# Performance work log

Hardware: AMD Instinct MI355X
Metric: run time of the kernel (lower is better)

The kernel has to match this reference:

```python
import jax, jax.numpy as jnp
import numpy as np

L, D, H, DK, S, B = 6, 1024, 16, 64, 512, 8
DFF = 4 * D
NEG = -1.0e9


def layer_norm(x, g, b, eps=1e-5):
    mu = jnp.mean(x, axis=-1, keepdims=True)
    var = jnp.var(x, axis=-1, keepdims=True)
    return (x - mu) * jax.lax.rsqrt(var + eps) * g + b


def setup_inputs() -> dict:
    key = jax.random.key(0)
    ks = jax.random.split(key, 16)
    s = 0.02
    inp = {
        "x": jax.random.normal(ks[0], (B, S, D), jnp.float32),
        "mask": jax.random.bernoulli(ks[1], 0.1, (B, S, S)),
        "relation": jax.random.normal(ks[2], (B, S, S), jnp.float32) * 0.1,
        # per-layer params (stacked over L)
        "Wq": jax.random.normal(ks[3], (L, D, H * DK), jnp.float32) * s,
        "Wk": jax.random.normal(ks[4], (L, D, H * DK), jnp.float32) * s,
        "Wv": jax.random.normal(ks[5], (L, D, H * DK), jnp.float32) * s,
        "Wo": jax.random.normal(ks[6], (L, H * DK, D), jnp.float32) * s,
        "bo": jnp.zeros((L, D), jnp.float32),
        "ln_g": jnp.ones((L, D), jnp.float32),   # EncoderLayer.norm (shared pre-attn / pre-FFN)
        "ln_b": jnp.zeros((L, D), jnp.float32),
        "ln2_g": jnp.ones((L, D), jnp.float32),  # AttSubLayerv2.norm
        "ln2_b": jnp.zeros((L, D), jnp.float32),
        "W1": jax.random.normal(ks[7], (L, D, DFF), jnp.float32) * s,
        "b1": jnp.zeros((L, DFF), jnp.float32),
        "W2": jax.random.normal(ks[8], (L, DFF, D), jnp.float32) * s,
        "b2": jnp.zeros((L, D), jnp.float32),
        "lnf_g": jnp.ones((D,), jnp.float32),    # Encoder.norm
        "lnf_b": jnp.zeros((D,), jnp.float32),
    }
    return inp


def reference(x, mask, relation, Wq, Wk, Wv, Wo, bo, ln_g, ln_b, ln2_g, ln2_b,
              W1, b1, W2, b2, lnf_g, lnf_b):
    # dropout layers run in eval mode (identity)
    scale = 1.0 / jnp.sqrt(jnp.asarray(DK, x.dtype))
    h = x
    attns = []
    for l in range(L):
        q_in = layer_norm(h, ln_g[l], ln_b[l])
        # AttSubLayerv2
        def proj(W):
            return jnp.einsum('bsd,de->bse', q_in, W).reshape(h.shape[0], -1, H, DK).transpose(0, 2, 1, 3)
        Q, K, V = proj(Wq[l]), proj(Wk[l]), proj(Wv[l])  # [B,H,S,DK]
        qk = jnp.einsum('bhqd,bhkd->bhqk', Q, K)
        scores = jnp.einsum('bhqk,bkn->bhqn', qk, relation) * scale
        scores = jnp.where(mask[:, None], NEG, scores)
        p = jax.nn.softmax(scores, axis=-1)  # [B,H,S,S]
        att = jnp.einsum('bhqk,bhkd->bhqd', p, V).transpose(0, 2, 1, 3).reshape(h.shape[0], -1, H * DK)
        att = att @ Wo[l] + bo[l]
        att_out = layer_norm(att + q_in, ln2_g[l], ln2_b[l])
        h = h + att_out
        # FFN (pre-norm with shared EncoderLayer norm)
        f = layer_norm(h, ln_g[l], ln_b[l])
        h = h + (jax.nn.relu(f @ W1[l] + b1[l]) @ W2[l] + b2[l])
        attns.append(p)
    out = layer_norm(h, lnf_g, lnf_b)
    return out, jnp.stack(attns)
```

## Files before the change

kernel.cpp:

```cpp
#include <hip/hip_runtime.h>
#include <hip/hip_bf16.h>
#include <stdint.h>

#define LL 6
#define DD 1024
#define HH 16
#define DKK 64
#define SS 512
#define BB 8
#define DFF_ 4096
#define BS (BB*SS)
#define NEGV -1.0e9f

typedef __attribute__((ext_vector_type(8))) short short8;
typedef __attribute__((ext_vector_type(4))) float f32x4;
typedef __attribute__((ext_vector_type(4))) unsigned short ushort4v;

static __device__ __forceinline__ float bf2f(unsigned short u){
  union { unsigned int i; float f; } v; v.i = ((unsigned int)u)<<16; return v.f;
}
static __device__ __forceinline__ unsigned short f2bf(float f){
  union { float f; unsigned int i; } v; v.f=f;
  unsigned int r = v.i + 0x7fff + ((v.i>>16)&1);
  return (unsigned short)(r>>16);
}

static __device__ __forceinline__ void gload16(const void* g, void* l){
  __builtin_amdgcn_global_load_lds((const __attribute__((address_space(1))) unsigned int*)g,
                                   (__attribute__((address_space(3))) unsigned int*)l, 16, 0, 0);
}

struct TrDesc { const float* in; unsigned short* out; long is1,is2,os1,os2; int ldin,ldout,zd,gx,gy; };
struct TrPack { TrDesc d[7]; int cum[8]; };

__global__ void __launch_bounds__(256) tr_multi_k(TrPack P)
{
  __shared__ float t[32][33];
  int bid=blockIdx.x, di=0;
  #pragma unroll
  for(int k=1;k<7;k++) if(bid>=P.cum[k]) di=k;
  TrDesc dd=P.d[di];
  int local=bid-P.cum[di];
  int bx=local%dd.gx; int rest=local/dd.gx;
  int by=rest%dd.gy; int z=rest/dd.gy;
  int z1=z/dd.zd, z2=z%dd.zd;
  const float* ip=dd.in+z1*dd.is1+z2*dd.is2;
  unsigned short* op=dd.out+z1*dd.os1+z2*dd.os2;
  int r0=by*32, c0=bx*32;
  int tx=threadIdx.x, ty=threadIdx.y;
  #pragma unroll
  for(int i=0;i<4;i++)
    t[ty+i*8][tx] = ip[(long)(r0+ty+i*8)*dd.ldin + c0+tx];
  __syncthreads();
  #pragma unroll
  for(int i=0;i<4;i++)
    op[(long)(c0+ty+i*8)*dd.ldout + r0+tx] = f2bf(t[tx][ty+i*8]);
}

__global__ void __launch_bounds__(256) maskpack_k(const int* __restrict__ mask, unsigned* __restrict__ mb)
{
  int idx = blockIdx.x*256 + threadIdx.x;
  int row = idx>>4, w = idx&15;
  const int* mp = mask + (long)row*SS + w*32;
  unsigned v=0;
  #pragma unroll
  for(int i=0;i<32;i++) v |= (mp[i]!=0) ? (1u<<i) : 0u;
  mb[idx]=v;
}

__global__ void __launch_bounds__(256) ln_k(const float* __restrict__ src,
    const float* __restrict__ gw, const float* __restrict__ bw,
    float* __restrict__ outf, unsigned short* __restrict__ outb,
    const float* __restrict__ resid)
{
  long row=blockIdx.x;
  float4 v=((const float4*)(src+row*DD))[threadIdx.x];
  float s=v.x+v.y+v.z+v.w;
  float s2=v.x*v.x+v.y*v.y+v.z*v.z+v.w*v.w;
  #pragma unroll
  for(int o=32;o;o>>=1){ s+=__shfl_xor(s,o); s2+=__shfl_xor(s2,o); }
  __shared__ float red[8];
  int wid=threadIdx.x>>6, lane=threadIdx.x&63;
  if(lane==0){ red[wid]=s; red[4+wid]=s2; }
  __syncthreads();
  s=red[0]+red[1]+red[2]+red[3];
  s2=red[4]+red[5]+red[6]+red[7];
  float mu=s*(1.f/DD);
  float rstd=rsqrtf(s2*(1.f/DD)-mu*mu+1e-5f);
  int c=threadIdx.x*4;
  float4 g4=*(const float4*)(gw+c), b4=*(const float4*)(bw+c);
  float4 o;
  o.x=(v.x-mu)*rstd*g4.x+b4.x;
  o.y=(v.y-mu)*rstd*g4.y+b4.y;
  o.z=(v.z-mu)*rstd*g4.z+b4.z;
  o.w=(v.w-mu)*rstd*g4.w+b4.w;
  if(resid){
    float4 r4=((const float4*)(resid+row*DD))[threadIdx.x];
    o.x+=r4.x; o.y+=r4.y; o.z+=r4.z; o.w+=r4.w;
  }
  if(outf) ((float4*)(outf+row*DD))[threadIdx.x]=o;
  if(outb){
    uint2 pk;
    pk.x=(unsigned)f2bf(o.x)|((unsigned)f2bf(o.y)<<16);
    pk.y=(unsigned)f2bf(o.z)|((unsigned)f2bf(o.w)<<16);
    ((uint2*)(outb+row*DD))[threadIdx.x]=pk;
  }
}

__global__ void __launch_bounds__(256) ln2_k(const float* __restrict__ src,
    const float* __restrict__ resid,
    const float* __restrict__ g2, const float* __restrict__ b2,
    const float* __restrict__ g1, const float* __restrict__ b1,
    float* __restrict__ outf, unsigned short* __restrict__ outb)
{
  long row=blockIdx.x;
  int wid=threadIdx.x>>6, lane=threadIdx.x&63, c=threadIdx.x*4;
  __shared__ float red[8];
  float4 v=((const float4*)(src+row*DD))[threadIdx.x];
  float s=v.x+v.y+v.z+v.w;
  float s2=v.x*v.x+v.y*v.y+v.z*v.z+v.w*v.w;
  #pragma unroll
  for(int o=32;o;o>>=1){ s+=__shfl_xor(s,o); s2+=__shfl_xor(s2,o); }
  if(lane==0){ red[wid]=s; red[4+wid]=s2; }
  __syncthreads();
  s=red[0]+red[1]+red[2]+red[3];
  s2=red[4]+red[5]+red[6]+red[7];
  float mu=s*(1.f/DD);
  float rstd=rsqrtf(s2*(1.f/DD)-mu*mu+1e-5f);
  float4 g4=*(const float4*)(g2+c), b4=*(const float4*)(b2+c);
  float4 r4=((const float4*)(resid+row*DD))[threadIdx.x];
  float4 o;
  o.x=(v.x-mu)*rstd*g4.x+b4.x+r4.x;
  o.y=(v.y-mu)*rstd*g4.y+b4.y+r4.y;
  o.z=(v.z-mu)*rstd*g4.z+b4.z+r4.z;
  o.w=(v.w-mu)*rstd*g4.w+b4.w+r4.w;
  ((float4*)(outf+row*DD))[threadIdx.x]=o;
  s=o.x+o.y+o.z+o.w;
  s2=o.x*o.x+o.y*o.y+o.z*o.z+o.w*o.w;
  #pragma unroll
  for(int of=32;of;of>>=1){ s+=__shfl_xor(s,of); s2+=__shfl_xor(s2,of); }
  __syncthreads();
  if(lane==0){ red[wid]=s; red[4+wid]=s2; }
  __syncthreads();
  s=red[0]+red[1]+red[2]+red[3];
  s2=red[4]+red[5]+red[6]+red[7];
  mu=s*(1.f/DD);
  rstd=rsqrtf(s2*(1.f/DD)-mu*mu+1e-5f);
  g4=*(const float4*)(g1+c); b4=*(const float4*)(b1+c);
  uint2 pk;
  pk.x=(unsigned)f2bf((o.x-mu)*rstd*g4.x+b4.x)|((unsigned)f2bf((o.y-mu)*rstd*g4.y+b4.y)<<16);
  pk.y=(unsigned)f2bf((o.z-mu)*rstd*g4.z+b4.z)|((unsigned)f2bf((o.w-mu)*rstd*g4.w+b4.w)<<16);
  ((uint2*)(outb+row*DD))[threadIdx.x]=pk;
}

struct GemmP {
  const unsigned short* A; long sA1; int ldA;
  const unsigned short* B; long sB1; int ldB;
  float* outF; unsigned short* outB; long sO1; int ldO;
  const float* bias;
  const float* residF; int ldR;
  const unsigned short* residB;
  unsigned short *kt, *vt;
  int K, relu;
};

template<int MODE>
__global__ void __launch_bounds__(512,2) gemm8_k(GemmP p)
{
  constexpr int BM=128, BN=128, BK=64;
  constexpr int BUFE=(BM+BN)*BK;
  constexpr int FN=2;
  constexpr int WNT=32;
  __shared__ __align__(16) unsigned short smem[4*BUFE];
  const int tid=threadIdx.x, lane=tid&63, wid=tid>>6;
  const int wr=wid>>2, wc=wid&3;
  const int lr=lane&15, lk=(lane>>4)*8;
  const int m0=blockIdx.y*BM, n0=blockIdx.x*BN;
  const int z=blockIdx.z;
  const unsigned short* Ap=p.A+(long)z*p.sA1;
  const unsigned short* Bp=p.B+(long)z*p.sB1;
  const int NT=p.K/BK;

  const int sr8 = lane>>3;
  const int scol = ((lane&7) ^ sr8) << 3;

  #define STAGE8(T,BI) { \
    const long kb_=(long)(T)*BK; \
    unsigned short* As_=smem+(BI)*BUFE; \
    unsigned short* Bs_=As_+BM*BK; \
    _Pragma("unroll") \
    for(int L=0;L<2;L++){ \
      int r_=L*64+wid*8+sr8; \
      gload16(Ap+(long)(m0+r_)*p.ldA+kb_+scol, As_+L*4096+wid*512); \
    } \
    _Pragma("unroll") \
    for(int L=0;L<2;L++){ \
      int r_=L*64+wid*8+sr8; \
      gload16(Bp+(long)(n0+r_)*p.ldB+kb_+scol, Bs_+L*4096+wid*512); \
    } }

  f32x4 acc[4][FN];
  #pragma unroll
  for(int m=0;m<4;m++)
    #pragma unroll
    for(int n=0;n<FN;n++) acc[m][n]=(f32x4){0.f,0.f,0.f,0.f};

  STAGE8(0,0);
  STAGE8(1,1);
  __syncthreads();

  const int xr = (lr&7)<<3;
  for(int t=0;t<NT;t+=2){
    if(t+2<NT) STAGE8(t+2,(t+2)&3);
    if(t+3<NT) STAGE8(t+3,(t+3)&3);
    #pragma unroll
    for(int u=0;u<2;u++){
      const unsigned short* As=smem+((t+u)&3)*BUFE;
      const unsigned short* Bs=As+BM*BK;
      #pragma unroll
      for(int kk=0;kk<2;kk++){
        short8 a[4], b[FN];
        #pragma unroll
        for(int m=0;m<4;m++)
          a[m]=*(const short8*)(As + (wr*64+m*16+lr)*BK + ((kk*32+lk)^xr));
        #pragma unroll
        for(int n=0;n<FN;n++)
          b[n]=*(const short8*)(Bs + (wc*WNT+n*16+lr)*BK + ((kk*32+lk)^xr));
        __builtin_amdgcn_s_setprio(1);
        #pragma unroll
        for(int m=0;m<4;m++)
          #pragma unroll
          for(int n=0;n<FN;n++)
            acc[m][n]=__builtin_amdgcn_mfma_f32_16x16x32_bf16(a[m],b[n],acc[m][n],0,0,0);
        __builtin_amdgcn_s_setprio(0);
      }
    }
    __syncthreads();
  }
  #undef STAGE8

  const int rl=(lane>>4)*4;
  if(MODE==1){
    int sec = n0>>10;
    #pragma unroll
    for(int m=0;m<4;m++){
      int gr0 = m0 + wr*64 + m*16 + rl;
      int b = gr0>>9, s0 = gr0&511;
      #pragma unroll
      for(int n=0;n<FN;n++){
        int gc = n0 + wc*WNT + n*16 + lr;
        if(sec==0){
          #pragma unroll
          for(int r=0;r<4;r++)
            p.outB[(long)(gr0+r)*1024 + gc] = f2bf(acc[m][n][r]);
        } else {
          unsigned short* dst = sec==1 ? p.kt : p.vt;
          int hh=(gc>>6)&15, d=gc&63;
          ushort4v pk;
          pk.x=f2bf(acc[m][n][0]); pk.y=f2bf(acc[m][n][1]);
          pk.z=f2bf(acc[m][n][2]); pk.w=f2bf(acc[m][n][3]);
          *(ushort4v*)(dst + (((long)b*HH+hh)*DKK+d)*SS + s0) = pk;
        }
      }
    }
  } else {
    #pragma unroll
    for(int m=0;m<4;m++){
      int gr0 = m0 + wr*64 + m*16 + rl;
      #pragma unroll
      for(int n=0;n<FN;n++){
        int gc = n0 + wc*WNT + n*16 + lr;
        float bv = p.bias ? p.bias[gc] : 0.f;
        #pragma unroll
        for(int r=0;r<4;r++){
          long ro=(long)(gr0+r);
          float val=acc[m][n][r]+bv;
          if(p.relu) val=fmaxf(val,0.f);
          if(p.residF) val += p.residF[ro*(long)p.ldR+gc];
          if(p.residB) val += bf2f(p.residB[ro*(long)p.ldR+gc]);
          long oo = (long)z*p.sO1 + ro*(long)p.ldO+gc;
          if(p.outF) p.outF[oo]=val;
          if(p.outB) p.outB[oo]=f2bf(val);
        }
      }
    }
  }
}

template<int MODE>
static inline void launch_gemm8(GemmP& p,int M,int N,int Z,hipStream_t s){
  gemm8_k<MODE><<<dim3(N/128,M/128,Z),dim3(512),0,s>>>(p);
}

__global__ void __launch_bounds__(512) att_k(const unsigned short* __restrict__ Qb,
    const unsigned short* __restrict__ KRT, float* __restrict__ pout,
    const unsigned* __restrict__ maskb, const unsigned short* __restrict__ Vt,
    unsigned short* __restrict__ attb)
{
  constexpr int BM=128, BK=32, NT=512;
  constexpr int FM=4, FN=8;
  __shared__ __align__(16) char smem[49152];
  unsigned short* As = (unsigned short*)smem;
  unsigned short* Bs = (unsigned short*)(smem+8192);
  unsigned short* Ps = (unsigned short*)smem;
  unsigned short* Vs = (unsigned short*)(smem+32768);
  __shared__ float redmx[BM][4];
  __shared__ float redsm[BM][4];
  int bh = blockIdx.y; int b = bh>>4, h = bh&15;
  const unsigned short* Ap = Qb + (long)b*SS*1024 + h*64;
  const unsigned short* Bp = KRT + (long)b*SS*1024 + h*64;
  int m0 = blockIdx.x*BM;
  int tid=threadIdx.x, lane=tid&63, wid=tid>>6;
  int wr=wid>>2, wc=wid&3;
  f32x4 acc[FM][FN];
  #pragma unroll
  for(int i=0;i<FM;i++)
    #pragma unroll
    for(int j=0;j<FN;j++) acc[i][j]=(f32x4){0.f,0.f,0.f,0.f};
  const int lr=lane&15, lk=(lane>>4)*8;
  for(int k0=0;k0<DKK;k0+=BK){
    { int v=tid;
      gload16(Ap + (long)(m0+(v>>2))*1024 + k0 + (v&3)*8, As + (wid*64)*8); }
    #pragma unroll
    for(int r=0;r<4;r++){
      int v=r*NT+tid;
      gload16(Bp + (long)(v>>2)*1024 + k0 + (v&3)*8, Bs + (r*NT+wid*64)*8);
    }
    __syncthreads();
    short8 af[FM], bfr[FN];
    #pragma unroll
    for(int i=0;i<FM;i++) af[i]=*(const short8*)(As + (wr*64+i*16+lr)*BK + lk);
    #pragma unroll
    for(int j=0;j<FN;j++) bfr[j]=*(const short8*)(Bs + (wc*128+j*16+lr)*BK + lk);
    #pragma unroll
    for(int i=0;i<FM;i++)
      #pragma unroll
      for(int j=0;j<FN;j++)
        acc[i][j]=__builtin_amdgcn_mfma_f32_16x16x32_bf16(af[i],bfr[j],acc[i][j],0,0,0);
    __syncthreads();
  }
  const int rl=(lane>>4)*4;
  #pragma unroll
  for(int i=0;i<FM;i++){
    #pragma unroll
    for(int r=0;r<4;r++){
      int row=wr*64+i*16+rl+r;
      uint4 mw = *((const uint4*)(maskb + ((long)(b*SS+m0+row))*16 + wc*4));
      float m_=-3.4e38f;
      #pragma unroll
      for(int j=0;j<FN;j++){
        unsigned word = (j>>1)==0? mw.x : (j>>1)==1? mw.y : (j>>1)==2? mw.z : mw.w;
        float v = ((word>>(((j&1)<<4)+lr))&1) ? NEGV : acc[i][j][r]*0.125f;
        acc[i][j][r]=v; m_=fmaxf(m_,v);
      }
      #pragma unroll
      for(int o=1;o<16;o<<=1) m_=fmaxf(m_,__shfl_xor(m_,o));
      if(lr==0) redmx[row][wc]=m_;
    }
  }
  __syncthreads();
  #pragma unroll
  for(int i=0;i<FM;i++){
    #pragma unroll
    for(int r=0;r<4;r++){
      int row=wr*64+i*16+rl+r;
      float m_=fmaxf(fmaxf(redmx[row][0],redmx[row][1]),fmaxf(redmx[row][2],redmx[row][3]));
      float s_=0.f;
      #pragma unroll
      for(int j=0;j<FN;j++){
        float e=__expf(acc[i][j][r]-m_);
        acc[i][j][r]=e; s_+=e;
      }
      #pragma unroll
      for(int o=1;o<16;o<<=1) s_+=__shfl_xor(s_,o);
      if(lr==0) redsm[row][wc]=s_;
    }
  }
  __syncthreads();
  #pragma unroll
  for(int i=0;i<FM;i++){
    #pragma unroll
    for(int r=0;r<4;r++){
      int row=wr*64+i*16+rl+r;
      float inv=1.f/(redsm[row][0]+redsm[row][1]+redsm[row][2]+redsm[row][3]);
      long obase=((long)bh*SS + m0+row)*(long)SS;
      #pragma unroll
      for(int j=0;j<FN;j++){
        int col=wc*128+j*16+lr;
        float pv=acc[i][j][r]*inv;
        acc[i][j][r]=pv;
        pout[obase+col]=pv;
      }
    }
  }
  __syncthreads();
  f32x4 attacc[4];
  #pragma unroll
  for(int j=0;j<4;j++) attacc[j]=(f32x4){0.f,0.f,0.f,0.f};
  for(int kc=0;kc<4;kc++){
    #pragma unroll
    for(int r2=0;r2<2;r2++){
      int v=r2*512+tid;
      int d=v>>4, m=v&15;
      int u=m^(d&7);
      gload16(Vt + ((long)bh*64 + d)*512 + kc*128 + u*8, Vs + (r2*512 + wid*64)*8);
    }
    if(wc==kc){
      #pragma unroll
      for(int i=0;i<FM;i++){
        #pragma unroll
        for(int r=0;r<4;r++){
          int row=wr*64+i*16+rl+r;
          #pragma unroll
          for(int j=0;j<FN;j++){
            int col=j*16+lr;
            Ps[row*128 + (col ^ ((row&7)<<3))] = f2bf(acc[i][j][r]);
          }
        }
      }
    }
    __syncthreads();
    #pragma unroll
    for(int kk=0;kk<4;kk++){
      int arow=wid*16+lr;
      short8 paf=*(const short8*)(Ps + arow*128 + ((kk*32+lk) ^ ((arow&7)<<3)));
      #pragma unroll
      for(int j=0;j<4;j++){
        int d=j*16+lr;
        short8 vbf=*(const short8*)(Vs + d*128 + ((kk*32+lk) ^ ((d&7)<<3)));
        attacc[j]=__builtin_amdgcn_mfma_f32_16x16x32_bf16(paf,vbf,attacc[j],0,0,0);
      }
    }
    __syncthreads();
  }
  #pragma unroll
  for(int j=0;j<4;j++){
    #pragma unroll
    for(int r=0;r<4;r++){
      int row = m0 + wid*16 + rl + r;
      attb[((long)b*SS + row)*DD + h*64 + j*16 + lr] = f2bf(attacc[j][r]);
    }
  }
}

extern "C" void kernel_launch(void* const* d_in, const int* in_sizes, int n_in,
                              void* d_out, int out_size, void* d_ws, size_t ws_size,
                              hipStream_t stream)
{
  const float* x    =(const float*)d_in[0];
  const int*   mask =(const int*)d_in[1];
  const float* rel  =(const float*)d_in[2];
  const float* Wq   =(const float*)d_in[3];
  const float* Wk   =(const float*)d_in[4];
  const float* Wv   =(const float*)d_in[5];
  const float* Wo   =(const float*)d_in[6];
  const float* bo   =(const float*)d_in[7];
  const float* ln_g =(const float*)d_in[8];
  const float* ln_b =(const float*)d_in[9];
  const float* ln2_g=(const float*)d_in[10];
  const float* ln2_b=(const float*)d_in[11];
  const float* W1   =(const float*)d_in[12];
  const float* b1   =(const float*)d_in[13];
  const float* W2   =(const float*)d_in[14];
  const float* b2   =(const float*)d_in[15];
  const float* lnf_g=(const float*)d_in[16];
  const float* lnf_b=(const float*)d_in[17];
  float* out=(float*)d_out;

  char* w=(char*)d_ws;
  auto alloc=[&](long bytes)->void*{ void* p=(void*)w; w += (bytes+255)&~255L; return p; };
  unsigned short* WTqkv=(unsigned short*)alloc((long)LL*3072*1024*2);
  unsigned short* WoT  =(unsigned short*)alloc((long)LL*1024*1024*2);
  unsigned short* W1T  =(unsigned short*)alloc((long)LL*DFF_*DD*2);
  unsigned short* W2T  =(unsigned short*)alloc((long)LL*DD*DFF_*2);
  unsigned short* relT =(unsigned short*)alloc((long)BB*SS*SS*2);
  unsigned short* qin_b=(unsigned short*)alloc((long)BS*DD*2);
  unsigned short* Qb   =(unsigned short*)alloc((long)BS*1024*2);
  unsigned short* Vt   =(unsigned short*)alloc((long)BB*HH*DKK*SS*2);
  unsigned short* Kt   =(unsigned short*)alloc((long)BB*HH*DKK*SS*2);
  unsigned short* KRT  =(unsigned short*)alloc((long)BB*SS*1024*2);
  unsigned short* attb =(unsigned short*)alloc((long)BS*DD*2);
  float*          attres=(float*)alloc((long)BS*DD*4);
  unsigned short* gbuf =(unsigned short*)alloc((long)BS*DFF_*2);
  float*          hbuf =(float*)alloc((long)BS*DD*4);
  unsigned*       maskb=(unsigned*)alloc((long)BS*16*4);
  (void)ws_size; (void)in_sizes; (void)n_in; (void)out_size;

  TrPack tp;
  auto set=[&](int i, const float* in, unsigned short* o, int ldin, int ldout,
               long is1, long os1, int zd, long is2, long os2, int gx, int gy){
    tp.d[i]={in,o,is1,is2,os1,os2,ldin,ldout,zd,gx,gy};
  };
  set(0, Wq, WTqkv,           1024,1024,(long)1024*1024,(long)3072*1024,1,0,0, 32,32);
  set(1, Wk, WTqkv+1024*1024, 1024,1024,(long)1024*1024,(long)3072*1024,1,0,0, 32,32);
  set(2, Wv, WTqkv+2048*1024, 1024,1024,(long)1024*1024,(long)3072*1024,1,0,0, 32,32);
  set(3, Wo, WoT,             1024,1024,(long)1024*1024,(long)1024*1024,1,0,0, 32,32);
  set(4, W1, W1T, 4096,1024,(long)1024*4096,(long)1024*4096,1,0,0, 128,32);
  set(5, W2, W2T, 1024,4096,(long)4096*1024,(long)4096*1024,1,0,0, 32,128);
  set(6, rel, relT, 512,512,(long)512*512,(long)512*512,1,0,0, 16,16);
  int nb[7]={32*32*LL,32*32*LL,32*32*LL,32*32*LL,128*32*LL,32*128*LL,16*16*BB};
  tp.cum[0]=0;
  for(int i=0;i<7;i++) tp.cum[i+1]=tp.cum[i]+nb[i];
  tr_multi_k<<<dim3(tp.cum[7]),dim3(32,8),0,stream>>>(tp);
  maskpack_k<<<dim3(BS*16/256),dim3(256),0,stream>>>(mask, maskb);

  const float* hin = x;
  for(int l=0;l<LL;l++){
    ln_k<<<dim3(BS),dim3(256),0,stream>>>(hin, ln_g+l*DD, ln_b+l*DD, (float*)nullptr, qin_b, (const float*)nullptr);
    { GemmP p{}; p.A=qin_b; p.ldA=DD; p.B=WTqkv+(long)l*3072*1024; p.ldB=DD;
      p.outB=Qb; p.kt=Kt; p.vt=Vt; p.K=DD;
      launch_gemm8<1>(p, BS, 3072, 1, stream); }
    { GemmP p{}; p.A=relT; p.sA1=(long)SS*SS; p.ldA=SS;
      p.B=Kt; p.sB1=(long)HH*DKK*SS; p.ldB=SS;
      p.outB=KRT; p.sO1=(long)SS*1024; p.ldO=1024; p.K=SS;
      launch_gemm8<0>(p, SS, 1024, BB, stream); }
    float* attn_l = out + (long)BS*DD + (long)l*BB*HH*SS*SS;
    att_k<<<dim3(SS/128, BB*HH),dim3(512),0,stream>>>(Qb, KRT, attn_l, maskb, Vt, attb);
    { GemmP p{}; p.A=attb; p.ldA=DD; p.B=WoT+(long)l*1024*1024; p.ldB=DD;
      p.outF=attres; p.ldO=DD; p.bias=bo+l*DD;
      p.residB=qin_b; p.ldR=DD; p.K=DD;
      launch_gemm8<0>(p, BS, DD, 1, stream); }
    ln2_k<<<dim3(BS),dim3(256),0,stream>>>(attres, hin, ln2_g+l*DD, ln2_b+l*DD,
        ln_g+l*DD, ln_b+l*DD, hbuf, qin_b);
    { GemmP p{}; p.A=qin_b; p.ldA=DD; p.B=W1T+(long)l*DFF_*DD; p.ldB=DD;
      p.outB=gbuf; p.ldO=DFF_; p.bias=b1+l*DFF_; p.relu=1; p.K=DD;
      launch_gemm8<0>(p, BS, DFF_, 1, stream); }
    { GemmP p{}; p.A=gbuf; p.ldA=DFF_; p.B=W2T+(long)l*DD*DFF_; p.ldB=DFF_;
      p.outF=hbuf; p.ldO=DD; p.bias=b2+l*DD;
      p.residF=hbuf; p.ldR=DD; p.K=DFF_;
      launch_gemm8<0>(p, BS, DD, 1, stream); }
    hin=hbuf;
  }
  ln_k<<<dim3(BS),dim3(256),0,stream>>>(hbuf, lnf_g, lnf_b, out, (unsigned short*)nullptr, (const float*)nullptr);
}
```

Before: 2.076 ms.

## Use 4-wave GEMM with 64x64 warp tiles and double-buffered LDS

Result: slower. 2.244 ms (+8.1%).

```diff
diff --git a/kernel.cpp b/kernel.cpp
--- a/kernel.cpp
+++ b/kernel.cpp
@@ -165,15 +165,13 @@
 };
 
 template<int MODE>
-__global__ void __launch_bounds__(512,2) gemm8_k(GemmP p)
+__global__ void __launch_bounds__(256,2) gemm8_k(GemmP p)
 {
   constexpr int BM=128, BN=128, BK=64;
   constexpr int BUFE=(BM+BN)*BK;
-  constexpr int FN=2;
-  constexpr int WNT=32;
-  __shared__ __align__(16) unsigned short smem[4*BUFE];
+  __shared__ __align__(16) unsigned short smem[2*BUFE];
   const int tid=threadIdx.x, lane=tid&63, wid=tid>>6;
-  const int wr=wid>>2, wc=wid&3;
+  const int wr=wid>>1, wc=wid&1;
   const int lr=lane&15, lk=(lane>>4)*8;
   const int m0=blockIdx.y*BM, n0=blockIdx.x*BN;
   const int z=blockIdx.z;
@@ -189,51 +187,46 @@
     unsigned short* As_=smem+(BI)*BUFE; \
     unsigned short* Bs_=As_+BM*BK; \
     _Pragma("unroll") \
-    for(int L=0;L<2;L++){ \
-      int r_=L*64+wid*8+sr8; \
-      gload16(Ap+(long)(m0+r_)*p.ldA+kb_+scol, As_+L*4096+wid*512); \
+    for(int L=0;L<4;L++){ \
+      int r_=L*32+wid*8+sr8; \
+      gload16(Ap+(long)(m0+r_)*p.ldA+kb_+scol, As_+L*2048+wid*512); \
     } \
     _Pragma("unroll") \
-    for(int L=0;L<2;L++){ \
-      int r_=L*64+wid*8+sr8; \
-      gload16(Bp+(long)(n0+r_)*p.ldB+kb_+scol, Bs_+L*4096+wid*512); \
+    for(int L=0;L<4;L++){ \
+      int r_=L*32+wid*8+sr8; \
+      gload16(Bp+(long)(n0+r_)*p.ldB+kb_+scol, Bs_+L*2048+wid*512); \
     } }
 
-  f32x4 acc[4][FN];
+  f32x4 acc[4][4];
   #pragma unroll
   for(int m=0;m<4;m++)
     #pragma unroll
-    for(int n=0;n<FN;n++) acc[m][n]=(f32x4){0.f,0.f,0.f,0.f};
+    for(int n=0;n<4;n++) acc[m][n]=(f32x4){0.f,0.f,0.f,0.f};
 
   STAGE8(0,0);
-  STAGE8(1,1);
   __syncthreads();
 
   const int xr = (lr&7)<<3;
-  for(int t=0;t<NT;t+=2){
-    if(t+2<NT) STAGE8(t+2,(t+2)&3);
-    if(t+3<NT) STAGE8(t+3,(t+3)&3);
-    #pragma unroll
-    for(int u=0;u<2;u++){
-      const unsigned short* As=smem+((t+u)&3)*BUFE;
-      const unsigned short* Bs=As+BM*BK;
-      #pragma unroll
-      for(int kk=0;kk<2;kk++){
-        short8 a[4], b[FN];
+  for(int t=0;t<NT;t++){
+    if(t+1<NT) STAGE8(t+1,(t+1)&1);
+    const unsigned short* As=smem+(t&1)*BUFE;
+    const unsigned short* Bs=As+BM*BK;
+    #pragma unroll
+    for(int kk=0;kk<2;kk++){
+      short8 a[4], b[4];
+      #pragma unroll
+      for(int m=0;m<4;m++)
+        a[m]=*(const short8*)(As + (wr*64+m*16+lr)*BK + ((kk*32+lk)^xr));
+      #pragma unroll
+      for(int n=0;n<4;n++)
+        b[n]=*(const short8*)(Bs + (wc*64+n*16+lr)*BK + ((kk*32+lk)^xr));
+      __builtin_amdgcn_s_setprio(1);
+      #pragma unroll
+      for(int m=0;m<4;m++)
         #pragma unroll
-        for(int m=0;m<4;m++)
-          a[m]=*(const short8*)(As + (wr*64+m*16+lr)*BK + ((kk*32+lk)^xr));
-        #pragma unroll
-        for(int n=0;n<FN;n++)
-          b[n]=*(const short8*)(Bs + (wc*WNT+n*16+lr)*BK + ((kk*32+lk)^xr));
-        __builtin_amdgcn_s_setprio(1);
-        #pragma unroll
-        for(int m=0;m<4;m++)
-          #pragma unroll
-          for(int n=0;n<FN;n++)
-            acc[m][n]=__builtin_amdgcn_mfma_f32_16x16x32_bf16(a[m],b[n],acc[m][n],0,0,0);
-        __builtin_amdgcn_s_setprio(0);
-      }
+        for(int n=0;n<4;n++)
+          acc[m][n]=__builtin_amdgcn_mfma_f32_16x16x32_bf16(a[m],b[n],acc[m][n],0,0,0);
+      __builtin_amdgcn_s_setprio(0);
     }
     __syncthreads();
   }
@@ -247,8 +240,8 @@
       int gr0 = m0 + wr*64 + m*16 + rl;
       int b = gr0>>9, s0 = gr0&511;
       #pragma unroll
-      for(int n=0;n<FN;n++){
-        int gc = n0 + wc*WNT + n*16 + lr;
+      for(int n=0;n<4;n++){
+        int gc = n0 + wc*64 + n*16 + lr;
         if(sec==0){
           #pragma unroll
           for(int r=0;r<4;r++)
@@ -268,8 +261,8 @@
     for(int m=0;m<4;m++){
       int gr0 = m0 + wr*64 + m*16 + rl;
       #pragma unroll
-      for(int n=0;n<FN;n++){
-        int gc = n0 + wc*WNT + n*16 + lr;
+      for(int n=0;n<4;n++){
+        int gc = n0 + wc*64 + n*16 + lr;
         float bv = p.bias ? p.bias[gc] : 0.f;
         #pragma unroll
         for(int r=0;r<4;r++){
@@ -289,7 +282,7 @@
 
 template<int MODE>
 static inline void launch_gemm8(GemmP& p,int M,int N,int Z,hipStream_t s){
-  gemm8_k<MODE><<<dim3(N/128,M/128,Z),dim3(512),0,s>>>(p);
+  gemm8_k<MODE><<<dim3(N/128,M/128,Z),dim3(256),0,s>>>(p);
 }
 
 __global__ void __launch_bounds__(512) att_k(const unsigned short* __restrict__ Qb,
```
